# Optimization experiments

Hardware: AMD Instinct MI355X
Metric: run time of the kernel (lower is better)

The kernel has to match this reference:

```python
import jax, jax.numpy as jnp
import numpy as np
from jax import lax

PATCH = 17
THRESH = 0.5


def _bbox_from_mask(mask_np):
    # mask_np: [D,H,W] bool. Matches mask_to_3d_bbox (min/max of nonzero coords).
    z, y, x = np.nonzero(mask_np)
    return (int(x.min()), int(y.min()), int(z.min()),
            int(x.max()), int(y.max()), int(z.max()))


def _extract_patches(vol, bbox):
    # vol: [1,1,D,H,W]; crop uses exclusive max (slice z_min:z_max) like the torch code
    x0, y0, z0, x1, y1, z1 = bbox
    t = vol[:, :, z0:z1, y0:y1, x0:x1]
    pads = []
    for d in t.shape[2:]:
        r = d % PATCH
        p = (PATCH - r) % PATCH
        pads.append((p // 2, p - p // 2))
    t = jnp.pad(t, ((0, 0), (0, 0), pads[0], pads[1], pads[2]))
    D, H, W = t.shape[2:]
    nD, nH, nW = D // PATCH, H // PATCH, W // PATCH
    p = t.reshape(nD, PATCH, nH, PATCH, nW, PATCH)
    p = p.transpose(0, 2, 4, 1, 3, 5).reshape(-1, PATCH, PATCH, PATCH)
    return p[:, None]  # [N,1,17,17,17]


def _conv3d(x, w, b, stride):
    y = lax.conv_general_dilated(x, w, (stride,) * 3, 'VALID',
                                 dimension_numbers=('NCDHW', 'OIDHW', 'NCDHW'))
    return y + b.reshape(1, -1, 1, 1, 1)


def _model(fixed, moving, c1w, c1b, c2w, c2b, f1w, f1b, f2w, f2b):
    # Stand-in for the opaque torch.jit model: siamese-concat 3D CNN -> MLP -> tanh.
    x = jnp.concatenate([fixed, moving], axis=1)          # [N,2,17,17,17]
    x = jax.nn.relu(_conv3d(x, c1w, c1b, 2))              # [N,32,8,8,8]
    x = jax.nn.relu(_conv3d(x, c2w, c2b, 2))              # [N,64,3,3,3]
    x = x.reshape(x.shape[0], -1)                         # [N,1728]
    x = jax.nn.relu(x @ f1w.T + f1b)                      # [N,256]
    return jnp.tanh(x @ f2w.T + f2b)                      # [N,1]


def setup_inputs() -> dict:
    key = jax.random.key(0)
    ks = jax.random.split(key, 10)
    V = 222
    source = jax.random.normal(ks[0], (1, 1, V, V, V), jnp.float32)
    target = jax.random.uniform(ks[1], (1, 1, V, V, V), jnp.float32)
    fc_in = 64 * 3 * 3 * 3
    return {
        'source': source,
        'target': target,
        'conv1_w': jax.random.normal(ks[2], (32, 2, 3, 3, 3), jnp.float32) * 0.1,
        'conv1_b': jnp.zeros((32,), jnp.float32),
        'conv2_w': jax.random.normal(ks[3], (64, 32, 3, 3, 3), jnp.float32) * 0.05,
        'conv2_b': jnp.zeros((64,), jnp.float32),
        'fc1_w': jax.random.normal(ks[4], (256, fc_in), jnp.float32) * 0.02,
        'fc1_b': jnp.zeros((256,), jnp.float32),
        'fc2_w': jax.random.normal(ks[5], (1, 256), jnp.float32) * 0.05,
        'fc2_b': jnp.zeros((1,), jnp.float32),
    }


def reference(source, target, conv1_w, conv1_b, conv2_w, conv2_b,
              fc1_w, fc1_b, fc2_w, fc2_b):
    mask_np = np.asarray(target) > 0
    bbox = _bbox_from_mask(mask_np.squeeze())
    fixed_patches = _extract_patches(target, bbox)   # [N,1,17,17,17]
    moving_patches = _extract_patches(source, bbox)
    # per-patch zero fraction on fixed patches; keep if <= threshold
    zero_frac = jnp.mean((fixed_patches[:, 0] == 0).astype(jnp.float32), axis=(1, 2, 3))
    keep = (zero_frac <= THRESH).astype(jnp.float32)  # [N]
    out = _model(fixed_patches, moving_patches, conv1_w, conv1_b, conv2_w, conv2_b,
                 fc1_w, fc1_b, fc2_w, fc2_b)          # [N,1]
    # mean over kept patches == weighted mean (stream-compaction-free, same math)
    return jnp.sum(out[:, 0] * keep) / jnp.sum(keep)
```

## Files before the change

### kernel.cpp

```cpp
#include <hip/hip_runtime.h>


template <bool USE_W1T>
static __device__ __forceinline__ float2 dmr15_patch(
    int p, int t,
    const float* __restrict__ src, const float* __restrict__ tgt,
    const float* __restrict__ c1w, const float* __restrict__ c1b,
    const float* __restrict__ c2w, const float* __restrict__ c2b,
    const float* __restrict__ fw,  const float* __restrict__ f1b,
    const float* __restrict__ f2w, const float* __restrict__ f2b,
    float* __restrict__ sBuf, float* __restrict__ sRed) {
  int pd = p / 169; int rem = p - pd * 169; int phh = rem / 13; int pww = rem - phh * 13;
  int z0 = pd * 17, y0 = phh * 17, x0 = pww * 17;

  int wv  = t >> 6;
  int od  = (t >> 3) & 7, oh = t & 7;
  int oc2 = t & 63;

  float cnt = 0.f;
  for (int idx = t; idx < 4913; idx += 256) {
    int a = idx / 289; int r2 = idx - a * 289; int b = r2 / 17; int c = r2 - b * 17;
    float v = tgt[((size_t)(z0 + a) * 222 + (y0 + b)) * 222 + (x0 + c)];
    sBuf[idx] = v;
    if (v == 0.0f) cnt += 1.f;
  }
  sRed[t] = cnt;
  __syncthreads();
  for (int o = 128; o > 0; o >>= 1) {
    if (t < o) sRed[t] += sRed[t + o];
    __syncthreads();
  }
  float keep = (sRed[0] / 4913.0f <= 0.5f) ? 1.0f : 0.0f;
  __syncthreads();

  float acc2[27];
  #pragma unroll
  for (int i = 0; i < 27; i++) acc2[i] = 0.f;

  #pragma unroll 1
  for (int half = 0; half < 2; half++) {
    float acc[4][8];
    #pragma unroll
    for (int i = 0; i < 4; i++)
      #pragma unroll
      for (int j = 0; j < 8; j++) acc[i][j] = 0.f;

    #pragma unroll 1
    for (int ic = 0; ic < 2; ic++) {
      if (half + ic > 0) {
        const float* vol = ic ? src : tgt;
        __syncthreads();
        for (int idx = t; idx < 4913; idx += 256) {
          int a = idx / 289; int r2 = idx - a * 289; int b = r2 / 17; int c = r2 - b * 17;
          sBuf[idx] = vol[((size_t)(z0 + a) * 222 + (y0 + b)) * 222 + (x0 + c)];
        }
        __syncthreads();
      }
      #pragma unroll 1
      for (int td = 0; td < 3; td++) {
        #pragma unroll 1
        for (int th = 0; th < 3; th++) {
          int rbase = (2 * od + td) * 289 + (2 * oh + th) * 17;
          float a[17];
          #pragma unroll
          for (int x = 0; x < 17; x++) a[x] = sBuf[rbase + x];
          #pragma unroll
          for (int ocr = 0; ocr < 4; ocr++) {
            int oc = half * 16 + wv * 4 + ocr;
            const float* wp = c1w + oc * 54 + ic * 27 + td * 9 + th * 3;
            float w0 = wp[0], w1 = wp[1], w2 = wp[2];
            #pragma unroll
            for (int ow = 0; ow < 8; ow++)
              acc[ocr][ow] += a[2 * ow] * w0 + a[2 * ow + 1] * w1 + a[2 * ow + 2] * w2;
          }
        }
      }
    }
    __syncthreads();
    #pragma unroll
    for (int ocr = 0; ocr < 4; ocr++) {
      int lo = wv * 4 + ocr;
      float b = c1b[half * 16 + lo];
      int base = lo * 512 + od * 64 + oh * 8;
      #pragma unroll
      for (int ow = 0; ow < 8; ow++)
        sBuf[base + ow] = fmaxf(acc[ocr][ow] + b, 0.f);
    }
    __syncthreads();

    #pragma unroll 1
    for (int icr = 0; icr < 4; icr++) {
      int icl = wv * 4 + icr;
      int ic  = half * 16 + icl;
      const float* cbase = sBuf + icl * 512;
      #pragma unroll 1
      for (int td = 0; td < 3; td++) {
        #pragma unroll 1
        for (int th = 0; th < 3; th++) {
          const float* wp = c2w + oc2 * 864 + ic * 27 + td * 9 + th * 3;
          float w0 = wp[0], w1 = wp[1], w2 = wp[2];
          #pragma unroll
          for (int zo = 0; zo < 3; zo++) {
            #pragma unroll
            for (int yo = 0; yo < 3; yo++) {
              const float* rp = cbase + (2 * zo + td) * 64 + (2 * yo + th) * 8;
              #pragma unroll
              for (int xo = 0; xo < 3; xo++)
                acc2[zo * 9 + yo * 3 + xo] +=
                    rp[2 * xo] * w0 + rp[2 * xo + 1] * w1 + rp[2 * xo + 2] * w2;
            }
          }
        }
      }
    }
  }
  __syncthreads();
  #pragma unroll
  for (int pos = 0; pos < 27; pos++)
    sBuf[(wv * 27 + pos) * 64 + oc2] = acc2[pos];
  __syncthreads();
  for (int idx = t; idx < 1728; idx += 256) {
    int o = idx & 63, pos = idx >> 6;
    float v = sBuf[pos * 64 + o] + sBuf[(27 + pos) * 64 + o] +
              sBuf[(54 + pos) * 64 + o] + sBuf[(81 + pos) * 64 + o];
    sBuf[pos * 64 + o] = fmaxf(v + c2b[o], 0.f);
  }
  __syncthreads();

  float acc1 = 0.f;
  if (USE_W1T) {
    const float* wcol = fw + t;
    #pragma unroll 2
    for (int o = 0; o < 64; o++) {
      #pragma unroll
      for (int pos = 0; pos < 27; pos++)
        acc1 += sBuf[pos * 64 + o] * wcol[(size_t)(o * 27 + pos) * 256];
    }
  } else {
    const float* frow = fw + (size_t)t * 1728;
    #pragma unroll 4
    for (int o = 0; o < 64; o++) {
      const float* fo = frow + o * 27;
      #pragma unroll
      for (int pos = 0; pos < 27; pos++)
        acc1 += sBuf[pos * 64 + o] * fo[pos];
    }
  }
  float h = fmaxf(acc1 + f1b[t], 0.f);
  sRed[t] = h * f2w[t];
  __syncthreads();
  for (int o = 128; o > 0; o >>= 1) {
    if (t < o) sRed[t] += sRed[t + o];
    __syncthreads();
  }
  float2 rk;
  rk.x = tanhf(sRed[0] + f2b[0]) * keep;
  rk.y = keep;
  __syncthreads();
  return rk;
}

__global__ void dmr15_tr(const float* __restrict__ f1w, float* __restrict__ w1t) {
  int k = blockIdx.x;
  int n = threadIdx.x;
  w1t[(size_t)k * 256 + n] = f1w[(size_t)n * 1728 + k];
}

template <bool USE_W1T>
__global__ __launch_bounds__(256, 4)
void dmr15_hot(const float* __restrict__ src, const float* __restrict__ tgt,
               const float* __restrict__ c1w, const float* __restrict__ c1b,
               const float* __restrict__ c2w, const float* __restrict__ c2b,
               const float* __restrict__ fw,  const float* __restrict__ f1b,
               const float* __restrict__ f2w, const float* __restrict__ f2b,
               float* __restrict__ pr, float* __restrict__ pk) {
  __shared__ float sBuf[8192];
  __shared__ float sRed[256];
  int t = threadIdx.x;
  float2 rk = dmr15_patch<USE_W1T>(blockIdx.x, t, src, tgt, c1w, c1b, c2w, c2b,
                                   fw, f1b, f2w, f2b, sBuf, sRed);
  if (t == 0) { pr[blockIdx.x] = rk.x; pk[blockIdx.x] = rk.y; }
}

__global__ __launch_bounds__(256, 4)
void DMMRLoss_52621939310662_kernel(
    const float* __restrict__ src, const float* __restrict__ tgt,
    const float* __restrict__ c1w, const float* __restrict__ c1b,
    const float* __restrict__ c2w, const float* __restrict__ c2b,
    const float* __restrict__ w1t, const float* __restrict__ f1b,
    const float* __restrict__ f2w, const float* __restrict__ f2b,
    float* __restrict__ pr, float* __restrict__ pk) {
  __shared__ float sBuf[8192];
  __shared__ float sRed[256];
  int t = threadIdx.x;
  float2 rk = dmr15_patch<true>(blockIdx.x, t, src, tgt, c1w, c1b, c2w, c2b,
                                w1t, f1b, f2w, f2b, sBuf, sRed);
  if (t == 0) { pr[blockIdx.x] = rk.x; pk[blockIdx.x] = rk.y; }
}

__global__ void dmr15_reduce(const float* __restrict__ pr, const float* __restrict__ pk,
                             float* __restrict__ out) {
  __shared__ float s1[256], s2[256];
  int t = threadIdx.x;
  float a = 0.f, b = 0.f;
  for (int p = t; p < 2197; p += 256) { a += pr[p]; b += pk[p]; }
  s1[t] = a; s2[t] = b;
  __syncthreads();
  for (int o = 128; o > 0; o >>= 1) {
    if (t < o) { s1[t] += s1[t + o]; s2[t] += s2[t + o]; }
    __syncthreads();
  }
  if (t == 0) out[0] = s1[0] / s2[0];
}

__global__ __launch_bounds__(256, 4)
void dmr15_solo(const float* __restrict__ src, const float* __restrict__ tgt,
                const float* __restrict__ c1w, const float* __restrict__ c1b,
                const float* __restrict__ c2w, const float* __restrict__ c2b,
                const float* __restrict__ f1w, const float* __restrict__ f1b,
                const float* __restrict__ f2w, const float* __restrict__ f2b,
                float* __restrict__ out) {
  __shared__ float sBuf[8192];
  __shared__ float sRed[256];
  __shared__ float sAcc[2];
  int t = threadIdx.x;
  if (t == 0) { sAcc[0] = 0.f; sAcc[1] = 0.f; }
  for (int p = 0; p < 2197; p++) {
    __syncthreads();
    float2 rk = dmr15_patch<false>(p, t, src, tgt, c1w, c1b, c2w, c2b,
                                   f1w, f1b, f2w, f2b, sBuf, sRed);
    if (t == 0) { sAcc[0] += rk.x; sAcc[1] += rk.y; }
  }
  __syncthreads();
  if (t == 0) out[0] = sAcc[0] / sAcc[1];
}

extern "C" void kernel_launch(void* const* d_in, const int* in_sizes, int n_in,
                              void* d_out, int out_size, void* d_ws, size_t ws_size,
                              hipStream_t stream) {
  const float* src = (const float*)d_in[0];
  const float* tgt = (const float*)d_in[1];
  const float* c1w = (const float*)d_in[2];
  const float* c1b = (const float*)d_in[3];
  const float* c2w = (const float*)d_in[4];
  const float* c2b = (const float*)d_in[5];
  const float* f1w = (const float*)d_in[6];
  const float* f1b = (const float*)d_in[7];
  const float* f2w = (const float*)d_in[8];
  const float* f2b = (const float*)d_in[9];
  float* out = (float*)d_out;

  const size_t nPK  = 2 * 2197;
  const size_t nW1T = 442368;
  if (d_ws && ws_size >= (nPK + nW1T) * sizeof(float)) {
    float* pr  = (float*)d_ws;
    float* pk  = pr + 2197;
    float* w1t = pr + nPK;
    dmr15_tr<<<1728, 256, 0, stream>>>(f1w, w1t);
    DMMRLoss_52621939310662_kernel<<<2197, 256, 0, stream>>>(
        src, tgt, c1w, c1b, c2w, c2b, w1t, f1b, f2w, f2b, pr, pk);
    dmr15_reduce<<<1, 256, 0, stream>>>(pr, pk, out);
  } else if (d_ws && ws_size >= nPK * sizeof(float)) {
    float* pr = (float*)d_ws;
    float* pk = pr + 2197;
    dmr15_hot<false><<<2197, 256, 0, stream>>>(
        src, tgt, c1w, c1b, c2w, c2b, f1w, f1b, f2w, f2b, pr, pk);
    dmr15_reduce<<<1, 256, 0, stream>>>(pr, pk, out);
  } else {
    dmr15_solo<<<1, 256, 0, stream>>>(
        src, tgt, c1w, c1b, c2w, c2b, f1w, f1b, f2w, f2b, out);
  }
}
```

Before: 470.8 us.

## Pad shared-memory patch layouts and pack FC1 weights as float4

Pads the shared-memory layouts of the input patch (row stride 25, plane stride 433) and the conv1 output (channel stride 528, depth stride 66) so that strided reads fall into different LDS banks. The conv2 output is stored in a separate region in the o*27+pos order that FC1 expects. FC1 weights are transposed into float4 groups so each thread issues 128-bit coalesced loads and reads its activations as float4 broadcasts. The cost is slightly more shared memory per block (8704 floats), which could affect occupancy.

Result: faster. 437.8 us (-7.0%).

```diff
diff --git a/kernel.cpp b/kernel.cpp
--- a/kernel.cpp
+++ b/kernel.cpp
@@ -1,8 +1,14 @@
 #include <hip/hip_runtime.h>
 
 
-template <bool USE_W1T>
-static __device__ __forceinline__ float2 dmr15_patch(
+static constexpr int kPS = 433;
+static constexpr int kRS = 25;
+static constexpr int kCS = 528;
+static constexpr int kZS = 66;
+static constexpr int kHOff = 6912;
+
+template <bool PACKED>
+static __device__ __forceinline__ float2 dmr16_patch(
     int p, int t,
     const float* __restrict__ src, const float* __restrict__ tgt,
     const float* __restrict__ c1w, const float* __restrict__ c1b,
@@ -21,7 +27,7 @@
   for (int idx = t; idx < 4913; idx += 256) {
     int a = idx / 289; int r2 = idx - a * 289; int b = r2 / 17; int c = r2 - b * 17;
     float v = tgt[((size_t)(z0 + a) * 222 + (y0 + b)) * 222 + (x0 + c)];
-    sBuf[idx] = v;
+    sBuf[a * kPS + b * kRS + c] = v;
     if (v == 0.0f) cnt += 1.f;
   }
   sRed[t] = cnt;
@@ -52,7 +58,8 @@
         __syncthreads();
         for (int idx = t; idx < 4913; idx += 256) {
           int a = idx / 289; int r2 = idx - a * 289; int b = r2 / 17; int c = r2 - b * 17;
-          sBuf[idx] = vol[((size_t)(z0 + a) * 222 + (y0 + b)) * 222 + (x0 + c)];
+          sBuf[a * kPS + b * kRS + c] =
+              vol[((size_t)(z0 + a) * 222 + (y0 + b)) * 222 + (x0 + c)];
         }
         __syncthreads();
       }
@@ -60,7 +67,7 @@
       for (int td = 0; td < 3; td++) {
         #pragma unroll 1
         for (int th = 0; th < 3; th++) {
-          int rbase = (2 * od + td) * 289 + (2 * oh + th) * 17;
+          int rbase = (2 * od + td) * kPS + (2 * oh + th) * kRS;
           float a[17];
           #pragma unroll
           for (int x = 0; x < 17; x++) a[x] = sBuf[rbase + x];
@@ -81,7 +88,7 @@
     for (int ocr = 0; ocr < 4; ocr++) {
       int lo = wv * 4 + ocr;
       float b = c1b[half * 16 + lo];
-      int base = lo * 512 + od * 64 + oh * 8;
+      int base = lo * kCS + od * kZS + oh * 8;
       #pragma unroll
       for (int ow = 0; ow < 8; ow++)
         sBuf[base + ow] = fmaxf(acc[ocr][ow] + b, 0.f);
@@ -92,7 +99,7 @@
     for (int icr = 0; icr < 4; icr++) {
       int icl = wv * 4 + icr;
       int ic  = half * 16 + icl;
-      const float* cbase = sBuf + icl * 512;
+      const float* cbase = sBuf + icl * kCS;
       #pragma unroll 1
       for (int td = 0; td < 3; td++) {
         #pragma unroll 1
@@ -103,7 +110,7 @@
           for (int zo = 0; zo < 3; zo++) {
             #pragma unroll
             for (int yo = 0; yo < 3; yo++) {
-              const float* rp = cbase + (2 * zo + td) * 64 + (2 * yo + th) * 8;
+              const float* rp = cbase + (2 * zo + td) * kZS + (2 * yo + th) * 8;
               #pragma unroll
               for (int xo = 0; xo < 3; xo++)
                 acc2[zo * 9 + yo * 3 + xo] +=
@@ -119,32 +126,29 @@
   for (int pos = 0; pos < 27; pos++)
     sBuf[(wv * 27 + pos) * 64 + oc2] = acc2[pos];
   __syncthreads();
+  float* sH = sBuf + kHOff;
   for (int idx = t; idx < 1728; idx += 256) {
     int o = idx & 63, pos = idx >> 6;
     float v = sBuf[pos * 64 + o] + sBuf[(27 + pos) * 64 + o] +
               sBuf[(54 + pos) * 64 + o] + sBuf[(81 + pos) * 64 + o];
-    sBuf[pos * 64 + o] = fmaxf(v + c2b[o], 0.f);
+    sH[o * 27 + pos] = fmaxf(v + c2b[o], 0.f);
   }
   __syncthreads();
 
   float acc1 = 0.f;
-  if (USE_W1T) {
-    const float* wcol = fw + t;
-    #pragma unroll 2
-    for (int o = 0; o < 64; o++) {
-      #pragma unroll
-      for (int pos = 0; pos < 27; pos++)
-        acc1 += sBuf[pos * 64 + o] * wcol[(size_t)(o * 27 + pos) * 256];
+  if (PACKED) {
+    const float4* w4p = (const float4*)fw;
+    const float4* sH4 = (const float4*)sH;
+    #pragma unroll 8
+    for (int k4 = 0; k4 < 432; k4++) {
+      float4 w  = w4p[k4 * 256 + t];
+      float4 hv = sH4[k4];
+      acc1 += w.x * hv.x + w.y * hv.y + w.z * hv.z + w.w * hv.w;
     }
   } else {
     const float* frow = fw + (size_t)t * 1728;
-    #pragma unroll 4
-    for (int o = 0; o < 64; o++) {
-      const float* fo = frow + o * 27;
-      #pragma unroll
-      for (int pos = 0; pos < 27; pos++)
-        acc1 += sBuf[pos * 64 + o] * fo[pos];
-    }
+    #pragma unroll 8
+    for (int k = 0; k < 1728; k++) acc1 += sH[k] * frow[k];
   }
   float h = fmaxf(acc1 + f1b[t], 0.f);
   sRed[t] = h * f2w[t];
@@ -160,26 +164,13 @@
   return rk;
 }
 
-__global__ void dmr15_tr(const float* __restrict__ f1w, float* __restrict__ w1t) {
-  int k = blockIdx.x;
-  int n = threadIdx.x;
-  w1t[(size_t)k * 256 + n] = f1w[(size_t)n * 1728 + k];
-}
-
-template <bool USE_W1T>
-__global__ __launch_bounds__(256, 4)
-void dmr15_hot(const float* __restrict__ src, const float* __restrict__ tgt,
-               const float* __restrict__ c1w, const float* __restrict__ c1b,
-               const float* __restrict__ c2w, const float* __restrict__ c2b,
-               const float* __restrict__ fw,  const float* __restrict__ f1b,
-               const float* __restrict__ f2w, const float* __restrict__ f2b,
-               float* __restrict__ pr, float* __restrict__ pk) {
-  __shared__ float sBuf[8192];
-  __shared__ float sRed[256];
-  int t = threadIdx.x;
-  float2 rk = dmr15_patch<USE_W1T>(blockIdx.x, t, src, tgt, c1w, c1b, c2w, c2b,
-                                   fw, f1b, f2w, f2b, sBuf, sRed);
-  if (t == 0) { pr[blockIdx.x] = rk.x; pk[blockIdx.x] = rk.y; }
+__global__ void dmr16_tr(const float* __restrict__ f1w, float* __restrict__ w1t4) {
+  int k4 = blockIdx.x;
+  int n  = threadIdx.x;
+  const float* s = f1w + (size_t)n * 1728 + k4 * 4;
+  float4 w;
+  w.x = s[0]; w.y = s[1]; w.z = s[2]; w.w = s[3];
+  ((float4*)w1t4)[k4 * 256 + n] = w;
 }
 
 __global__ __launch_bounds__(256, 4)
@@ -187,18 +178,33 @@
     const float* __restrict__ src, const float* __restrict__ tgt,
     const float* __restrict__ c1w, const float* __restrict__ c1b,
     const float* __restrict__ c2w, const float* __restrict__ c2b,
-    const float* __restrict__ w1t, const float* __restrict__ f1b,
+    const float* __restrict__ w1t4, const float* __restrict__ f1b,
     const float* __restrict__ f2w, const float* __restrict__ f2b,
     float* __restrict__ pr, float* __restrict__ pk) {
-  __shared__ float sBuf[8192];
+  __shared__ float sBuf[8704];
   __shared__ float sRed[256];
   int t = threadIdx.x;
-  float2 rk = dmr15_patch<true>(blockIdx.x, t, src, tgt, c1w, c1b, c2w, c2b,
-                                w1t, f1b, f2w, f2b, sBuf, sRed);
+  float2 rk = dmr16_patch<true>(blockIdx.x, t, src, tgt, c1w, c1b, c2w, c2b,
+                                w1t4, f1b, f2w, f2b, sBuf, sRed);
   if (t == 0) { pr[blockIdx.x] = rk.x; pk[blockIdx.x] = rk.y; }
 }
 
-__global__ void dmr15_reduce(const float* __restrict__ pr, const float* __restrict__ pk,
+__global__ __launch_bounds__(256, 4)
+void dmr16_hot_raw(const float* __restrict__ src, const float* __restrict__ tgt,
+                   const float* __restrict__ c1w, const float* __restrict__ c1b,
+                   const float* __restrict__ c2w, const float* __restrict__ c2b,
+                   const float* __restrict__ f1w, const float* __restrict__ f1b,
+                   const float* __restrict__ f2w, const float* __restrict__ f2b,
+                   float* __restrict__ pr, float* __restrict__ pk) {
+  __shared__ float sBuf[8704];
+  __shared__ float sRed[256];
+  int t = threadIdx.x;
+  float2 rk = dmr16_patch<false>(blockIdx.x, t, src, tgt, c1w, c1b, c2w, c2b,
+                                 f1w, f1b, f2w, f2b, sBuf, sRed);
+  if (t == 0) { pr[blockIdx.x] = rk.x; pk[blockIdx.x] = rk.y; }
+}
+
+__global__ void dmr16_reduce(const float* __restrict__ pr, const float* __restrict__ pk,
                              float* __restrict__ out) {
   __shared__ float s1[256], s2[256];
   int t = threadIdx.x;
@@ -214,20 +220,20 @@
 }
 
 __global__ __launch_bounds__(256, 4)
-void dmr15_solo(const float* __restrict__ src, const float* __restrict__ tgt,
+void dmr16_solo(const float* __restrict__ src, const float* __restrict__ tgt,
                 const float* __restrict__ c1w, const float* __restrict__ c1b,
                 const float* __restrict__ c2w, const float* __restrict__ c2b,
                 const float* __restrict__ f1w, const float* __restrict__ f1b,
                 const float* __restrict__ f2w, const float* __restrict__ f2b,
                 float* __restrict__ out) {
-  __shared__ float sBuf[8192];
+  __shared__ float sBuf[8704];
   __shared__ float sRed[256];
   __shared__ float sAcc[2];
   int t = threadIdx.x;
   if (t == 0) { sAcc[0] = 0.f; sAcc[1] = 0.f; }
   for (int p = 0; p < 2197; p++) {
     __syncthreads();
-    float2 rk = dmr15_patch<false>(p, t, src, tgt, c1w, c1b, c2w, c2b,
+    float2 rk = dmr16_patch<false>(p, t, src, tgt, c1w, c1b, c2w, c2b,
                                    f1w, f1b, f2w, f2b, sBuf, sRed);
     if (t == 0) { sAcc[0] += rk.x; sAcc[1] += rk.y; }
   }
@@ -250,24 +256,24 @@
   const float* f2b = (const float*)d_in[9];
   float* out = (float*)d_out;
 
+  const size_t nW1T = 442368;
   const size_t nPK  = 2 * 2197;
-  const size_t nW1T = 442368;
-  if (d_ws && ws_size >= (nPK + nW1T) * sizeof(float)) {
-    float* pr  = (float*)d_ws;
-    float* pk  = pr + 2197;
-    float* w1t = pr + nPK;
-    dmr15_tr<<<1728, 256, 0, stream>>>(f1w, w1t);
+  if (d_ws && ws_size >= (nW1T + nPK) * sizeof(float)) {
+    float* w1t4 = (float*)d_ws;
+    float* pr   = w1t4 + nW1T;
+    float* pk   = pr + 2197;
+    dmr16_tr<<<432, 256, 0, stream>>>(f1w, w1t4);
     DMMRLoss_52621939310662_kernel<<<2197, 256, 0, stream>>>(
-        src, tgt, c1w, c1b, c2w, c2b, w1t, f1b, f2w, f2b, pr, pk);
-    dmr15_reduce<<<1, 256, 0, stream>>>(pr, pk, out);
+        src, tgt, c1w, c1b, c2w, c2b, w1t4, f1b, f2w, f2b, pr, pk);
+    dmr16_reduce<<<1, 256, 0, stream>>>(pr, pk, out);
   } else if (d_ws && ws_size >= nPK * sizeof(float)) {
     float* pr = (float*)d_ws;
     float* pk = pr + 2197;
-    dmr15_hot<false><<<2197, 256, 0, stream>>>(
+    dmr16_hot_raw<<<2197, 256, 0, stream>>>(
         src, tgt, c1w, c1b, c2w, c2b, f1w, f1b, f2w, f2b, pr, pk);
-    dmr15_reduce<<<1, 256, 0, stream>>>(pr, pk, out);
+    dmr16_reduce<<<1, 256, 0, stream>>>(pr, pk, out);
   } else {
-    dmr15_solo<<<1, 256, 0, stream>>>(
+    dmr16_solo<<<1, 256, 0, stream>>>(
         src, tgt, c1w, c1b, c2w, c2b, f1w, f1b, f2w, f2b, out);
   }
 }
```
